# Kernel tuning notes

Measured on AMD Instinct MI355X. Metric: run time of the kernel, lower is better.

Reference implementation:

```python
import jax, jax.numpy as jnp
import numpy as np

DIM = 1024
DIM_HEAD = 64
N_HEADS = 16
CTX = 2048
BATCH = 4
EPS = 1e-5


def _alibi_M(ctx, n_heads):
    # head_scalars = 2**(-8/n) for n = [n_heads, ..., 1]
    scalars = 2.0 ** (-8.0 / np.arange(n_heads, 0, -1, dtype=np.float64))
    idx = np.arange(ctx)
    dist = -np.abs(idx[:, None] - idx[None, :]).astype(np.float64)  # [ctx, ctx]
    return jnp.asarray(scalars[:, None, None] * dist[None], dtype=jnp.float32)  # [h, ctx, ctx]


def setup_inputs() -> dict:
    key = jax.random.key(0)
    ks = jax.random.split(key, 6)
    inner = DIM_HEAD * N_HEADS
    s = 1.0 / np.sqrt(DIM)
    return {
        "x": jax.random.normal(ks[0], (BATCH, CTX, DIM), dtype=jnp.float32),
        "ln_w": jnp.ones((DIM,), dtype=jnp.float32),
        "ln_b": jnp.zeros((DIM,), dtype=jnp.float32),
        "Wq": jax.random.normal(ks[1], (DIM, inner), dtype=jnp.float32) * s,
        "Wk": jax.random.normal(ks[2], (DIM, inner), dtype=jnp.float32) * s,
        "Wv": jax.random.normal(ks[3], (DIM, inner), dtype=jnp.float32) * s,
        "Wo": jax.random.normal(ks[4], (inner, DIM), dtype=jnp.float32) * s,
        "M": _alibi_M(CTX, N_HEADS),
    }


def reference(x, ln_w, ln_b, Wq, Wk, Wv, Wo, M):
    # LayerNorm
    mu = jnp.mean(x, axis=-1, keepdims=True)
    var = jnp.mean(jnp.square(x - mu), axis=-1, keepdims=True)
    xn = (x - mu) * jax.lax.rsqrt(var + EPS) * ln_w + ln_b

    b, n, _ = xn.shape

    def heads(t):  # [b, n, h*d] -> [b, h, n, d]
        return t.reshape(b, n, N_HEADS, DIM_HEAD).transpose(0, 2, 1, 3)

    q = heads(xn @ Wq)
    k = heads(xn @ Wk)
    v = heads(xn @ Wv)

    scores = jnp.einsum("bhid,bhjd->bhij", q, k) / jnp.sqrt(jnp.float32(DIM_HEAD))
    scores = scores + M[None, :, :n, :n]  # ALiBi bias
    attn = jax.nn.softmax(scores, axis=-1)

    out = jnp.einsum("bhij,bhjd->bhid", attn, v)
    out = out.transpose(0, 2, 1, 3).reshape(b, n, N_HEADS * DIM_HEAD)
    return out @ Wo
```

## Files before the change

### kernel.cpp

```cpp
#include <hip/hip_runtime.h>

using s16x8  = __attribute__((ext_vector_type(8)))  short;
using s16x4  = __attribute__((ext_vector_type(4)))  short;
using f32x4  = __attribute__((ext_vector_type(4)))  float;
using f32x16 = __attribute__((ext_vector_type(16))) float;
using u32 = unsigned int;

#define LOG2E  1.4426950408889634f
#define QSCALE 0.18033688011112042f

static __device__ __forceinline__ ushort f2bf(float f) {
    union { float f; unsigned u; } c; c.f = f;
    unsigned u = c.u;
    unsigned r = (u + 0x7fffu + ((u >> 16) & 1u)) >> 16;
    return (ushort)r;
}
static __device__ __forceinline__ float bf2f(ushort h) {
    union { unsigned u; float f; } c; c.u = ((unsigned)h) << 16;
    return c.f;
}
static __device__ __forceinline__ u32 cvt_pk_bf16(float a, float b) {
    u32 r;
    asm("v_cvt_pk_bf16_f32 %0, %1, %2" : "=v"(r) : "v"(a), "v"(b));
    return r;
}
static __device__ __forceinline__ void permlane32_swap(u32& a, u32& b) {
    asm volatile("v_permlane32_swap_b32 %0, %1" : "+v"(a), "+v"(b));
}
static __device__ __forceinline__ f32x16 mfma32(s16x8 a, s16x8 b, f32x16 c) {
    return __builtin_amdgcn_mfma_f32_32x32x16_bf16(a, b, c, 0, 0, 0);
}
typedef __attribute__((address_space(3))) void lds_vt;
typedef __attribute__((address_space(1))) const void glb_vt;
static __device__ __forceinline__ void gload16(const void* g, void* l) {
    __builtin_amdgcn_global_load_lds((glb_vt*)g, (lds_vt*)l, 16, 0, 0);
}

#define PACKFRAG(p, base, out) {                              \
    u32 a0 = cvt_pk_bf16(p[base+0], p[base+1]);               \
    u32 b0 = cvt_pk_bf16(p[base+4], p[base+5]);               \
    permlane32_swap(a0, b0);                                  \
    u32 a1 = cvt_pk_bf16(p[base+2], p[base+3]);               \
    u32 b1 = cvt_pk_bf16(p[base+6], p[base+7]);               \
    permlane32_swap(a1, b1);                                  \
    union { u32 u[4]; s16x8 v; } f_;                          \
    f_.u[0] = a0; f_.u[1] = a1; f_.u[2] = b0; f_.u[3] = b1;   \
    out = f_.v; }

__global__ __launch_bounds__(256) void prep_kernel(const float* __restrict__ x,
                                                   const float* __restrict__ lnw,
                                                   const float* __restrict__ lnb,
                                                   const float* __restrict__ W0,
                                                   const float* __restrict__ W1,
                                                   const float* __restrict__ W2,
                                                   const float* __restrict__ W3,
                                                   ushort* __restrict__ wqkv,
                                                   ushort* __restrict__ wot,
                                                   ushort* __restrict__ xn) {
    __shared__ float tile[32][33];
    __shared__ float red[8];
    const int bid = blockIdx.x;
    if (bid < 4096) {
        const int z = bid >> 10, rem = bid & 1023;
        const float* W = (z == 0) ? W0 : (z == 1) ? W1 : (z == 2) ? W2 : W3;
        ushort* Wt = (z < 3) ? (wqkv + ((size_t)z << 20)) : wot;
        const float scale = (z == 0) ? QSCALE : 1.0f;
        const int k0 = (rem >> 5) * 32, n0 = (rem & 31) * 32;
        const int tx = threadIdx.x & 31, ty = threadIdx.x >> 5;
        #pragma unroll
        for (int i = 0; i < 32; i += 8)
            tile[ty + i][tx] = W[(size_t)(k0 + ty + i) * 1024 + n0 + tx];
        __syncthreads();
        #pragma unroll
        for (int i = 0; i < 32; i += 8)
            Wt[(size_t)(n0 + ty + i) * 1024 + k0 + tx] = f2bf(tile[tx][ty + i] * scale);
    } else {
        const int row = bid - 4096;
        const float4 v = ((const float4*)(x + (size_t)row * 1024))[threadIdx.x];
        float s  = v.x + v.y + v.z + v.w;
        float s2 = v.x * v.x + v.y * v.y + v.z * v.z + v.w * v.w;
        #pragma unroll
        for (int off = 1; off < 64; off <<= 1) {
            s  += __shfl_xor(s, off);
            s2 += __shfl_xor(s2, off);
        }
        const int wid = threadIdx.x >> 6, lane = threadIdx.x & 63;
        if (lane == 0) { red[wid] = s; red[4 + wid] = s2; }
        __syncthreads();
        s  = red[0] + red[1] + red[2] + red[3];
        s2 = red[4] + red[5] + red[6] + red[7];
        const float mu = s * (1.0f / 1024.0f);
        const float var = s2 * (1.0f / 1024.0f) - mu * mu;
        const float rstd = rsqrtf(var + 1e-5f);
        const float4 wv = ((const float4*)lnw)[threadIdx.x];
        const float4 bv = ((const float4*)lnb)[threadIdx.x];
        s16x4 o;
        o[0] = (short)f2bf((v.x - mu) * rstd * wv.x + bv.x);
        o[1] = (short)f2bf((v.y - mu) * rstd * wv.y + bv.y);
        o[2] = (short)f2bf((v.z - mu) * rstd * wv.z + bv.z);
        o[3] = (short)f2bf((v.w - mu) * rstd * wv.w + bv.w);
        ((s16x4*)xn)[(size_t)row * 256 + threadIdx.x] = o;
    }
}

__global__ __launch_bounds__(256) void gemm_kernel(const ushort* __restrict__ A,
                                                   const ushort* __restrict__ Wt,
                                                   ushort* __restrict__ oq,
                                                   float* __restrict__ of,
                                                   int nblkn, int omode) {
    __shared__ __align__(16) char glds[32768];

    const int nwg = gridDim.x;
    const int cpx = nwg >> 3;
    const int bid = blockIdx.x;
    const int logical = (bid & 7) * cpx + (bid >> 3);
    const int mb = logical / nblkn, nb = logical % nblkn;
    const int m0 = mb * 128, n0 = nb * 128;

    const int wid = threadIdx.x >> 6, lane = threadIdx.x & 63;
    const int l15 = lane & 15, lg = lane >> 4;
    const int wm = (wid >> 1) * 64, wn = (wid & 1) * 64;

    const int trow = threadIdx.x >> 2;
    const int tchk = threadIdx.x & 3;
    const ushort* ga0 = A  + (size_t)(m0 + trow) * 1024 + tchk * 8;
    const ushort* ga1 = ga0 + 64 * 1024;
    const ushort* gb0 = Wt + (size_t)(n0 + trow) * 1024 + tchk * 8;
    const ushort* gb1 = gb0 + 64 * 1024;
    char* lA = glds + wid * 1024;
    char* lB = glds + 8192 + wid * 1024;

#define GSTAGE(kk, bb) { \
        const int o_ = (bb) * 16384; \
        gload16(ga0 + (kk), lA + o_); \
        gload16(ga1 + (kk), lA + o_ + 4096); \
        gload16(gb0 + (kk), lB + o_); \
        gload16(gb1 + (kk), lB + o_ + 4096); \
    }

    f32x4 acc[4][4] = {};
    GSTAGE(0, 0);
    for (int k0 = 0; k0 < 1024; k0 += 32) {
        const int cur = (k0 >> 5) & 1;
        if (k0 < 992) {
            GSTAGE(k0 + 32, cur ^ 1);
            asm volatile("s_waitcnt vmcnt(4)" ::: "memory");
        } else {
            asm volatile("s_waitcnt vmcnt(0)" ::: "memory");
        }
        asm volatile("s_barrier" ::: "memory");

        const char* As = glds + cur * 16384;
        const char* Bs = As + 8192;
        s16x8 af[4], bf[4];
        #pragma unroll
        for (int mi = 0; mi < 4; ++mi)
            af[mi] = *(const s16x8*)(As + (wm + mi * 16 + l15) * 64 + lg * 16);
        #pragma unroll
        for (int ni = 0; ni < 4; ++ni)
            bf[ni] = *(const s16x8*)(Bs + (wn + ni * 16 + l15) * 64 + lg * 16);
        __builtin_amdgcn_s_setprio(1);
        #pragma unroll
        for (int mi = 0; mi < 4; ++mi)
            #pragma unroll
            for (int ni = 0; ni < 4; ++ni)
                acc[mi][ni] = __builtin_amdgcn_mfma_f32_16x16x32_bf16(af[mi], bf[ni], acc[mi][ni], 0, 0, 0);
        __builtin_amdgcn_s_setprio(0);

        asm volatile("s_barrier" ::: "memory");
    }
#undef GSTAGE

    #pragma unroll
    for (int mi = 0; mi < 4; ++mi) {
        #pragma unroll
        for (int ni = 0; ni < 4; ++ni) {
            const int row = m0 + wm + mi * 16 + lg * 4;
            const int col = n0 + wn + ni * 16 + l15;
            if (omode == 0) {
                const int tcol = col >> 10;
                const int h = (col >> 6) & 15, d = col & 63;
                const int bb = row >> 11, i = row & 2047;
                const int bhv = bb * 16 + h;
                if (tcol == 0) {
                    ushort* o = oq + ((((size_t)bhv) * 2048 + i) * 64 + d);
                    #pragma unroll
                    for (int r = 0; r < 4; ++r) o[(size_t)r * 64] = f2bf(acc[mi][ni][r]);
                } else if (tcol == 1) {
                    const int tt = i >> 6, half = (i >> 5) & 1, l31 = i & 31;
                    const int c = d >> 4, hi2 = (d >> 3) & 1, e = d & 7;
                    ushort* o = oq + ((size_t)1 << 23)
                              + ((size_t)(bhv * 32 + tt)) * 8192
                              + half * 2048 + c * 512 + (hi2 * 32 + l31) * 8 + e;
                    #pragma unroll
                    for (int r = 0; r < 4; ++r) o[r * 8] = f2bf(acc[mi][ni][r]);
                } else {
                    const int tt = i >> 6, jc = (i >> 3) & 7, e0 = i & 7;
                    const int s2 = ((jc >> 2) << 1) | ((jc >> 1) & 1), hi2 = jc & 1;
                    const int half = d >> 5, l31 = d & 31;
                    ushort* o = oq + ((size_t)1 << 23)
                              + ((size_t)(bhv * 32 + tt)) * 8192 + 4096
                              + half * 2048 + s2 * 512 + (hi2 * 32 + l31) * 8 + e0;
                    s16x4 pk;
                    #pragma unroll
                    for (int r = 0; r < 4; ++r) pk[r] = (short)f2bf(acc[mi][ni][r]);
                    *(s16x4*)o = pk;
                }
            } else {
                #pragma unroll
                for (int r = 0; r < 4; ++r) of[(size_t)(row + r) * 1024 + col] = acc[mi][ni][r];
            }
        }
    }
}

__global__ __launch_bounds__(512, 4) void attn_kernel(const ushort* __restrict__ Q,
                                                      const ushort* __restrict__ KV,
                                                      ushort* __restrict__ O) {
    __shared__ __align__(16) char lds[32768];

    const int bid = blockIdx.x;
    const int logical = (bid & 7) * 64 + (bid >> 3);
    const int bh = logical >> 3;
    const int b = bh >> 4, h = bh & 15;
    const int q0 = (logical & 7) * 256;

    const int wid = threadIdx.x >> 6, lane = threadIdx.x & 63;
    const int l31 = lane & 31, hi = lane >> 5;
    const float slope2 = exp2f(-8.0f / (float)(16 - h)) * LOG2E;

    const ushort* Qh  = Q + (size_t)bh * (2048 * 64);
    const ushort* kvsp = KV + (size_t)bh * 262144 + (size_t)(wid * 64 + lane) * 8;
    char* sdst = lds + wid * 1024;

    const int qw = q0 + wid * 32;
    const int qi = qw + l31;
    const float qif = (float)qi;
    const float fq4 = (float)(qi - 4 * hi);

    s16x8 qf[4];
    #pragma unroll
    for (int c = 0; c < 4; ++c)
        qf[c] = *(const s16x8*)(Qh + (size_t)qi * 64 + c * 16 + hi * 8);

    const u32 hmask = hi ? 0u : 0xFFFFFFFFu;
    union { u32 u[4]; s16x8 v; } kxa, kxb;
    kxa.u[0] = cvt_pk_bf16((float)l31 - 32.f, (float)l31 - 32.f) & hmask;
    kxa.u[1] = 0x3F803F80u & hmask; kxa.u[2] = 0; kxa.u[3] = 0;
    kxb.u[0] = cvt_pk_bf16((float)l31, (float)l31) & hmask;
    kxb.u[1] = kxa.u[1]; kxb.u[2] = 0; kxb.u[3] = 0;
    const float s2h = bf2f(f2bf(slope2));
    const float s2l = slope2 - s2h;
    const u32 wpos = ((u32)f2bf(s2l) << 16) | (u32)f2bf(s2h);
    const u32 wneg = wpos ^ 0x80008000u;

    f32x16 oacc0 = {}, oacc1 = {};
    float lsum = 0.0f;

#define STAGE(tt, bb) { \
        const ushort* s_ = kvsp + (size_t)(tt) * 8192; \
        char* d_ = sdst + (bb) * 16384; \
        gload16(s_,        d_); \
        gload16(s_ + 4096, d_ + 8192); \
    }

    STAGE(0, 0);

    for (int t = 0; t < 32; ++t) {
        const int cur = t & 1;
        const int j0 = t * 64;

        if (t < 31) {
            STAGE(t + 1, cur ^ 1);
            asm volatile("s_waitcnt vmcnt(2)" ::: "memory");
        } else {
            asm volatile("s_waitcnt vmcnt(0)" ::: "memory");
        }
        asm volatile("s_barrier" ::: "memory");

        const char* Kl = lds + cur * 16384;

        s16x8 kf[8];
        #pragma unroll
        for (int c = 0; c < 4; ++c) {
            kf[c]     = *(const s16x8*)(Kl + c * 1024 + lane * 16);
            kf[4 + c] = *(const s16x8*)(Kl + 4096 + c * 1024 + lane * 16);
        }

        f32x16 sa0 = {}, sa1 = {};
        __builtin_amdgcn_s_setprio(1);
        #pragma unroll
        for (int c = 0; c < 4; ++c) {
            sa0 = mfma32(kf[c], qf[c], sa0);
            sa1 = mfma32(kf[4 + c], qf[c], sa1);
        }
        __builtin_amdgcn_s_setprio(0);

        const bool strad = (j0 > qw - 64) && (j0 < qw + 32);
        float ps = 0.0f;
        if (!strad) {
            const bool left = (j0 < qw);
            const float v = (left ? -slope2 : slope2) * (qif - (float)(j0 + 32));
            const u32 pk0 = cvt_pk_bf16(v, 0.f);
            union { u32 u; float f; } vh; vh.u = pk0 << 16;
            union { u32 u[4]; s16x8 v8; } qx;
            qx.u[0] = (left ? wpos : wneg) & hmask;
            qx.u[1] = cvt_pk_bf16(vh.f, v - vh.f) & hmask;
            qx.u[2] = 0; qx.u[3] = 0;
            sa0 = mfma32(kxa.v, qx.v8, sa0);
            sa1 = mfma32(kxb.v, qx.v8, sa1);
            #pragma unroll
            for (int r = 0; r < 16; ++r) {
                sa0[r] = __builtin_amdgcn_exp2f(sa0[r]);
                sa1[r] = __builtin_amdgcn_exp2f(sa1[r]);
                ps += sa0[r] + sa1[r];
            }
        } else {
            const float base0 = fq4 - (float)j0;
            #pragma unroll
            for (int r = 0; r < 16; ++r) {
                const float C = (float)((r & 3) + 8 * (r >> 2));
                sa0[r] = __builtin_amdgcn_exp2f(fmaf(-slope2, fabsf(base0 - C), sa0[r]));
                sa1[r] = __builtin_amdgcn_exp2f(fmaf(-slope2, fabsf(base0 - 32.f - C), sa1[r]));
                ps += sa0[r] + sa1[r];
            }
        }
        lsum += ps;

        s16x8 pb00, pb01, pb10, pb11;
        PACKFRAG(sa0, 0, pb00);  PACKFRAG(sa0, 8, pb01);
        PACKFRAG(sa1, 0, pb10);  PACKFRAG(sa1, 8, pb11);

        s16x8 vf[8];
        #pragma unroll
        for (int s2i = 0; s2i < 4; ++s2i) {
            vf[s2i]     = *(const s16x8*)(Kl + 8192 + s2i * 1024 + lane * 16);
            vf[4 + s2i] = *(const s16x8*)(Kl + 12288 + s2i * 1024 + lane * 16);
        }
        __builtin_amdgcn_s_setprio(1);
        #pragma unroll
        for (int s = 0; s < 2; ++s) {
            #pragma unroll
            for (int kc = 0; kc < 2; ++kc) {
                const s16x8 pw = (s == 0) ? (kc == 0 ? pb00 : pb01)
                                          : (kc == 0 ? pb10 : pb11);
                oacc0 = mfma32(vf[s * 2 + kc], pw, oacc0);
                oacc1 = mfma32(vf[4 + s * 2 + kc], pw, oacc1);
            }
        }
        __builtin_amdgcn_s_setprio(0);

        asm volatile("s_barrier" ::: "memory");
    }
#undef STAGE

    const float lt = lsum + __shfl_xor(lsum, 32);
    const float inv = 1.0f / lt;

    char* ep = lds + wid * 4096;
    __syncthreads();
    #pragma unroll
    for (int dt = 0; dt < 2; ++dt) {
        #pragma unroll
        for (int pr = 0; pr < 8; ++pr) {
            const float va = (dt ? oacc1[2 * pr] : oacc0[2 * pr]) * inv;
            const float vb = (dt ? oacc1[2 * pr + 1] : oacc0[2 * pr + 1]) * inv;
            const u32 w = cvt_pk_bf16(va, vb);
            const int d0 = dt * 32 + ((2 * pr) & 3) + 8 * (pr >> 1) + 4 * hi;
            const int byte = l31 * 128 + ((d0 * 2) ^ ((l31 & 7) << 4));
            *(u32*)(ep + byte) = w;
        }
    }
    #pragma unroll
    for (int rr = 0; rr < 4; ++rr) {
        const int row = (lane >> 3) + rr * 8;
        const int c16 = (lane & 7) ^ (row & 7);
        const s16x8 v = *(const s16x8*)(ep + row * 128 + c16 * 16);
        *(s16x8*)(O + ((size_t)(b * 2048 + qw + row)) * 1024 + h * 64 + (lane & 7) * 8) = v;
    }
}

extern "C" void kernel_launch(void* const* d_in, const int* in_sizes, int n_in,
                              void* d_out, int out_size, void* d_ws, size_t ws_size,
                              hipStream_t stream) {
    (void)in_sizes; (void)n_in; (void)out_size; (void)ws_size;
    const float* x   = (const float*)d_in[0];
    const float* lnw = (const float*)d_in[1];
    const float* lnb = (const float*)d_in[2];
    const float* Wq  = (const float*)d_in[3];
    const float* Wk  = (const float*)d_in[4];
    const float* Wv  = (const float*)d_in[5];
    const float* Wo  = (const float*)d_in[6];

    char* w = (char*)d_ws;
    ushort* xn   = (ushort*)(w);
    ushort* wqkv = (ushort*)(w + (16u << 20));
    ushort* wot  = (ushort*)(w + (22u << 20));
    ushort* Qb   = (ushort*)(w + (24u << 20));

    prep_kernel<<<dim3(12288), 256, 0, stream>>>(x, lnw, lnb, Wq, Wk, Wv, Wo, wqkv, wot, xn);

    gemm_kernel<<<dim3(1536), 256, 0, stream>>>(xn, wqkv, Qb, nullptr, 24, 0);

    attn_kernel<<<dim3(512), 512, 0, stream>>>(Qb, Qb + ((size_t)1 << 23), xn);

    gemm_kernel<<<dim3(512), 256, 0, stream>>>(xn, wot, nullptr, (float*)d_out, 8, 1);
}
```

Before: 205.3 us.

## Give each attention wave two 32-row query tiles to reuse K/V fragments

The attention block drops from 8 to 4 waves, and each wave now handles 64 query rows as two 32-row tiles. K and V fragments read from LDS are shared across both tiles, which halves LDS reads per MFMA. Each thread issues twice as many global-to-LDS loads per stage. The cost is higher register pressure from four score accumulators and four output accumulators, and fewer waves per CU to hide latency. Launch bounds change to (256,2).

```diff
diff --git a/kernel.cpp b/kernel.cpp
--- a/kernel.cpp
+++ b/kernel.cpp
@@ -214,7 +214,7 @@
     }
 }
 
-__global__ __launch_bounds__(512, 4) void attn_kernel(const ushort* __restrict__ Q,
+__global__ __launch_bounds__(256, 2) void attn_kernel(const ushort* __restrict__ Q,
                                                       const ushort* __restrict__ KV,
                                                       ushort* __restrict__ O) {
     __shared__ __align__(16) char lds[32768];
@@ -230,18 +230,21 @@
     const float slope2 = exp2f(-8.0f / (float)(16 - h)) * LOG2E;
 
     const ushort* Qh  = Q + (size_t)bh * (2048 * 64);
-    const ushort* kvsp = KV + (size_t)bh * 262144 + (size_t)(wid * 64 + lane) * 8;
+    const ushort* kvsp = KV + (size_t)bh * 262144 + (size_t)threadIdx.x * 8;
     char* sdst = lds + wid * 1024;
 
-    const int qw = q0 + wid * 32;
-    const int qi = qw + l31;
-    const float qif = (float)qi;
-    const float fq4 = (float)(qi - 4 * hi);
-
-    s16x8 qf[4];
+    const int qw = q0 + wid * 64;
+    const int qiA = qw + l31, qiB = qiA + 32;
+    const float qifA = (float)qiA, qifB = (float)qiB;
+    const float fq4A = (float)(qiA - 4 * hi);
+    const float fq4B = fq4A + 32.0f;
+
+    s16x8 qf[8];
     #pragma unroll
-    for (int c = 0; c < 4; ++c)
-        qf[c] = *(const s16x8*)(Qh + (size_t)qi * 64 + c * 16 + hi * 8);
+    for (int c = 0; c < 4; ++c) {
+        qf[c]     = *(const s16x8*)(Qh + (size_t)qiA * 64 + c * 16 + hi * 8);
+        qf[4 + c] = *(const s16x8*)(Qh + (size_t)qiB * 64 + c * 16 + hi * 8);
+    }
 
     const u32 hmask = hi ? 0u : 0xFFFFFFFFu;
     union { u32 u[4]; s16x8 v; } kxa, kxb;
@@ -254,14 +257,16 @@
     const u32 wpos = ((u32)f2bf(s2l) << 16) | (u32)f2bf(s2h);
     const u32 wneg = wpos ^ 0x80008000u;
 
-    f32x16 oacc0 = {}, oacc1 = {};
-    float lsum = 0.0f;
+    f32x16 oA0 = {}, oA1 = {}, oB0 = {}, oB1 = {};
+    float lsumA = 0.0f, lsumB = 0.0f;
 
 #define STAGE(tt, bb) { \
         const ushort* s_ = kvsp + (size_t)(tt) * 8192; \
         char* d_ = sdst + (bb) * 16384; \
         gload16(s_,        d_); \
+        gload16(s_ + 2048, d_ + 4096); \
         gload16(s_ + 4096, d_ + 8192); \
+        gload16(s_ + 6144, d_ + 12288); \
     }
 
     STAGE(0, 0);
@@ -272,7 +277,7 @@
 
         if (t < 31) {
             STAGE(t + 1, cur ^ 1);
-            asm volatile("s_waitcnt vmcnt(2)" ::: "memory");
+            asm volatile("s_waitcnt vmcnt(4)" ::: "memory");
         } else {
             asm volatile("s_waitcnt vmcnt(0)" ::: "memory");
         }
@@ -287,49 +292,72 @@
             kf[4 + c] = *(const s16x8*)(Kl + 4096 + c * 1024 + lane * 16);
         }
 
-        f32x16 sa0 = {}, sa1 = {};
+        f32x16 sA0 = {}, sA1 = {}, sB0 = {}, sB1 = {};
         __builtin_amdgcn_s_setprio(1);
         #pragma unroll
         for (int c = 0; c < 4; ++c) {
-            sa0 = mfma32(kf[c], qf[c], sa0);
-            sa1 = mfma32(kf[4 + c], qf[c], sa1);
+            sA0 = mfma32(kf[c], qf[c], sA0);
+            sA1 = mfma32(kf[4 + c], qf[c], sA1);
+            sB0 = mfma32(kf[c], qf[4 + c], sB0);
+            sB1 = mfma32(kf[4 + c], qf[4 + c], sB1);
         }
         __builtin_amdgcn_s_setprio(0);
 
-        const bool strad = (j0 > qw - 64) && (j0 < qw + 32);
-        float ps = 0.0f;
+        const bool strad = (j0 == qw);
+        float psA = 0.0f, psB = 0.0f;
         if (!strad) {
             const bool left = (j0 < qw);
-            const float v = (left ? -slope2 : slope2) * (qif - (float)(j0 + 32));
-            const u32 pk0 = cvt_pk_bf16(v, 0.f);
-            union { u32 u; float f; } vh; vh.u = pk0 << 16;
-            union { u32 u[4]; s16x8 v8; } qx;
-            qx.u[0] = (left ? wpos : wneg) & hmask;
-            qx.u[1] = cvt_pk_bf16(vh.f, v - vh.f) & hmask;
-            qx.u[2] = 0; qx.u[3] = 0;
-            sa0 = mfma32(kxa.v, qx.v8, sa0);
-            sa1 = mfma32(kxb.v, qx.v8, sa1);
+            const float sgn = left ? -slope2 : slope2;
+            const float vA = sgn * (qifA - (float)(j0 + 32));
+            const float vB = sgn * (qifB - (float)(j0 + 32));
+            const u32 wsl = (left ? wpos : wneg) & hmask;
+            union { u32 u[4]; s16x8 v8; } qxA, qxB;
+            {
+                const u32 pk0 = cvt_pk_bf16(vA, 0.f);
+                union { u32 u; float f; } vh; vh.u = pk0 << 16;
+                qxA.u[0] = wsl; qxA.u[1] = cvt_pk_bf16(vh.f, vA - vh.f) & hmask;
+                qxA.u[2] = 0; qxA.u[3] = 0;
+            }
+            {
+                const u32 pk0 = cvt_pk_bf16(vB, 0.f);
+                union { u32 u; float f; } vh; vh.u = pk0 << 16;
+                qxB.u[0] = wsl; qxB.u[1] = cvt_pk_bf16(vh.f, vB - vh.f) & hmask;
+                qxB.u[2] = 0; qxB.u[3] = 0;
+            }
+            sA0 = mfma32(kxa.v, qxA.v8, sA0);
+            sA1 = mfma32(kxb.v, qxA.v8, sA1);
+            sB0 = mfma32(kxa.v, qxB.v8, sB0);
+            sB1 = mfma32(kxb.v, qxB.v8, sB1);
             #pragma unroll
             for (int r = 0; r < 16; ++r) {
-                sa0[r] = __builtin_amdgcn_exp2f(sa0[r]);
-                sa1[r] = __builtin_amdgcn_exp2f(sa1[r]);
-                ps += sa0[r] + sa1[r];
+                sA0[r] = __builtin_amdgcn_exp2f(sA0[r]);
+                sA1[r] = __builtin_amdgcn_exp2f(sA1[r]);
+                sB0[r] = __builtin_amdgcn_exp2f(sB0[r]);
+                sB1[r] = __builtin_amdgcn_exp2f(sB1[r]);
+                psA += sA0[r] + sA1[r];
+                psB += sB0[r] + sB1[r];
             }
         } else {
-            const float base0 = fq4 - (float)j0;
+            const float baseA = fq4A - (float)j0;
+            const float baseB = fq4B - (float)j0;
             #pragma unroll
             for (int r = 0; r < 16; ++r) {
                 const float C = (float)((r & 3) + 8 * (r >> 2));
-                sa0[r] = __builtin_amdgcn_exp2f(fmaf(-slope2, fabsf(base0 - C), sa0[r]));
-                sa1[r] = __builtin_amdgcn_exp2f(fmaf(-slope2, fabsf(base0 - 32.f - C), sa1[r]));
-                ps += sa0[r] + sa1[r];
-            }
-        }
-        lsum += ps;
-
-        s16x8 pb00, pb01, pb10, pb11;
-        PACKFRAG(sa0, 0, pb00);  PACKFRAG(sa0, 8, pb01);
-        PACKFRAG(sa1, 0, pb10);  PACKFRAG(sa1, 8, pb11);
+                sA0[r] = __builtin_amdgcn_exp2f(fmaf(-slope2, fabsf(baseA - C), sA0[r]));
+                sA1[r] = __builtin_amdgcn_exp2f(fmaf(-slope2, fabsf(baseA - 32.f - C), sA1[r]));
+                sB0[r] = __builtin_amdgcn_exp2f(fmaf(-slope2, fabsf(baseB - C), sB0[r]));
+                sB1[r] = __builtin_amdgcn_exp2f(fmaf(-slope2, fabsf(baseB - 32.f - C), sB1[r]));
+                psA += sA0[r] + sA1[r];
+                psB += sB0[r] + sB1[r];
+            }
+        }
+        lsumA += psA; lsumB += psB;
+
+        s16x8 pA0, pA1, pA2, pA3, pB0, pB1, pB2, pB3;
+        PACKFRAG(sA0, 0, pA0);  PACKFRAG(sA0, 8, pA1);
+        PACKFRAG(sA1, 0, pA2);  PACKFRAG(sA1, 8, pA3);
+        PACKFRAG(sB0, 0, pB0);  PACKFRAG(sB0, 8, pB1);
+        PACKFRAG(sB1, 0, pB2);  PACKFRAG(sB1, 8, pB3);
 
         s16x8 vf[8];
         #pragma unroll
@@ -342,10 +370,12 @@
         for (int s = 0; s < 2; ++s) {
             #pragma unroll
             for (int kc = 0; kc < 2; ++kc) {
-                const s16x8 pw = (s == 0) ? (kc == 0 ? pb00 : pb01)
-                                          : (kc == 0 ? pb10 : pb11);
-                oacc0 = mfma32(vf[s * 2 + kc], pw, oacc0);
-                oacc1 = mfma32(vf[4 + s * 2 + kc], pw, oacc1);
+                const s16x8 pwA = (s == 0) ? (kc == 0 ? pA0 : pA1) : (kc == 0 ? pA2 : pA3);
+                const s16x8 pwB = (s == 0) ? (kc == 0 ? pB0 : pB1) : (kc == 0 ? pB2 : pB3);
+                oA0 = mfma32(vf[s * 2 + kc], pwA, oA0);
+                oA1 = mfma32(vf[4 + s * 2 + kc], pwA, oA1);
+                oB0 = mfma32(vf[s * 2 + kc], pwB, oB0);
+                oB1 = mfma32(vf[4 + s * 2 + kc], pwB, oB1);
             }
         }
         __builtin_amdgcn_s_setprio(0);
@@ -354,25 +384,28 @@
     }
 #undef STAGE
 
-    const float lt = lsum + __shfl_xor(lsum, 32);
-    const float inv = 1.0f / lt;
-
-    char* ep = lds + wid * 4096;
+    const float ltA = lsumA + __shfl_xor(lsumA, 32);
+    const float ltB = lsumB + __shfl_xor(lsumB, 32);
+    const float invA = 1.0f / ltA, invB = 1.0f / ltB;
+
+    char* ep = lds + wid * 8192;
     __syncthreads();
     #pragma unroll
     for (int dt = 0; dt < 2; ++dt) {
         #pragma unroll
         for (int pr = 0; pr < 8; ++pr) {
-            const float va = (dt ? oacc1[2 * pr] : oacc0[2 * pr]) * inv;
-            const float vb = (dt ? oacc1[2 * pr + 1] : oacc0[2 * pr + 1]) * inv;
-            const u32 w = cvt_pk_bf16(va, vb);
             const int d0 = dt * 32 + ((2 * pr) & 3) + 8 * (pr >> 1) + 4 * hi;
-            const int byte = l31 * 128 + ((d0 * 2) ^ ((l31 & 7) << 4));
-            *(u32*)(ep + byte) = w;
+            const int swz = (d0 * 2) ^ ((l31 & 7) << 4);
+            const float vaA = (dt ? oA1[2 * pr] : oA0[2 * pr]) * invA;
+            const float vbA = (dt ? oA1[2 * pr + 1] : oA0[2 * pr + 1]) * invA;
+            *(u32*)(ep + l31 * 128 + swz) = cvt_pk_bf16(vaA, vbA);
+            const float vaB = (dt ? oB1[2 * pr] : oB0[2 * pr]) * invB;
+            const float vbB = (dt ? oB1[2 * pr + 1] : oB0[2 * pr + 1]) * invB;
+            *(u32*)(ep + (32 + l31) * 128 + swz) = cvt_pk_bf16(vaB, vbB);
         }
     }
     #pragma unroll
-    for (int rr = 0; rr < 4; ++rr) {
+    for (int rr = 0; rr < 8; ++rr) {
         const int row = (lane >> 3) + rr * 8;
         const int c16 = (lane & 7) ^ (row & 7);
         const s16x8 v = *(const s16x8*)(ep + row * 128 + c16 * 16);
@@ -402,7 +435,7 @@
 
     gemm_kernel<<<dim3(1536), 256, 0, stream>>>(xn, wqkv, Qb, nullptr, 24, 0);
 
-    attn_kernel<<<dim3(512), 512, 0, stream>>>(Qb, Qb + ((size_t)1 << 23), xn);
+    attn_kernel<<<dim3(512), 256, 0, stream>>>(Qb, Qb + ((size_t)1 << 23), xn);
 
     gemm_kernel<<<dim3(512), 256, 0, stream>>>(xn, wot, nullptr, (float*)d_out, 8, 1);
 }
```

After: 230.6 us. 1.12x slower.
